# Kernel optimization log

Hardware: AMD Instinct MI355X
Metric: run time of the kernel (lower is better)

The kernel has to match this reference:

```python
import jax, jax.numpy as jnp
import numpy as np
from itertools import combinations

EPS = 1e-5

# flattened channel-pair index list: 36 pairs of the 9 GLCM shift channels -> 72 indices
PAIRS = np.asarray(list(combinations(range(9), 2)), dtype=np.int32).reshape(-1)


def glcm_stack(img):
    # img: [B,1,H,W]; replicate torch slice+cat shifts exactly (edge rows/cols duplicated)
    left = lambda a: jnp.concatenate([a[:, :, :, 1:], a[:, :, :, -1:]], axis=3)
    up = lambda a: jnp.concatenate([a[:, :, 1:, :], a[:, :, -1:, :]], axis=2)
    down = lambda a: jnp.concatenate([a[:, :, :1, :], a[:, :, :-1, :]], axis=2)
    right = lambda a: jnp.concatenate([a[:, :, :, :1], a[:, :, :, :-1]], axis=3)
    gl3, gl6, gl7, gl8 = left(img), up(img), down(img), down(img)
    return jnp.concatenate([
        img, left(img), up(img), up(gl3), right(img),
        down(img), left(gl6), left(gl7), right(gl8)], axis=1)  # [B,9,H,W]


def bn(x, gamma, beta, mean, var):
    scale = (gamma / jnp.sqrt(var + EPS))[:, None, None]
    return (x - mean[:, None, None]) * scale + beta[:, None, None]


def setup_inputs() -> dict:
    key = jax.random.key(0)
    ks = jax.random.split(key, 8)
    n = 36
    x = jax.random.normal(ks[0], (32, 64, 224, 224), dtype=jnp.float32)
    gw = jax.random.normal(ks[1], (n, 2), dtype=jnp.float32) * 0.5      # grouped 1x1 conv [out=n, in/group=2]
    w1 = jax.random.normal(ks[2], (n, n), dtype=jnp.float32) * 0.1      # 1x1 conv n->n
    ca_w1 = jax.random.normal(ks[3], (n // 2, n), dtype=jnp.float32) * 0.2
    ca_w2 = jax.random.normal(ks[4], (n, n // 2), dtype=jnp.float32) * 0.2
    bng_g = jnp.ones((n,), jnp.float32); bng_b = jnp.zeros((n,), jnp.float32)
    bng_m = jax.random.normal(ks[5], (n,), dtype=jnp.float32) * 0.1
    bng_v = jnp.abs(jax.random.normal(ks[6], (n,), dtype=jnp.float32)) + 0.5
    bn1_g = jnp.ones((n,), jnp.float32); bn1_b = jnp.zeros((n,), jnp.float32)
    bn1_m = jax.random.normal(ks[7], (n,), dtype=jnp.float32) * 0.1
    bn1_v = jnp.ones((n,), jnp.float32)
    return dict(x=x, gw=gw, w1=w1, ca_w1=ca_w1, ca_w2=ca_w2,
                bng_g=bng_g, bng_b=bng_b, bng_m=bng_m, bng_v=bng_v,
                bn1_g=bn1_g, bn1_b=bn1_b, bn1_m=bn1_m, bn1_v=bn1_v)


def reference(x, gw, w1, ca_w1, ca_w2, bng_g, bng_b, bng_m, bng_v,
              bn1_g, bn1_b, bn1_m, bn1_v):
    avgout = jnp.mean(x, axis=1, keepdims=True)            # [B,1,H,W]
    g = glcm_stack(avgout)                                 # [B,9,H,W]
    B, _, H, W = g.shape
    feas = jnp.take(g, jnp.asarray(PAIRS), axis=1)         # [B,72,H,W]
    feas = feas.reshape(B, 36, 2, H, W)
    y = jnp.einsum('bgchw,gc->bghw', feas, gw)             # grouped 1x1 conv
    y = jax.nn.relu(bn(y, bng_g, bng_b, bng_m, bng_v))
    y = jnp.einsum('bchw,oc->bohw', y, w1)                 # 1x1 conv n->n
    y = bn(y, bn1_g, bn1_b, bn1_m, bn1_v)
    pooled = jnp.mean(y, axis=(2, 3))                      # [B,36]
    att = jax.nn.sigmoid(jax.nn.relu(pooled @ ca_w1.T) @ ca_w2.T)  # [B,36]
    y = y * att[:, :, None, None]
    out = jax.nn.sigmoid(jnp.sum(y, axis=1, keepdims=True))  # [B,1,H,W]
    return out
```

## Files before the change

### kernel.cpp

```cpp
#include <hip/hip_runtime.h>
#include <math.h>

#define B_   32
#define C_   64
#define H_   224
#define W_   224
#define HW_  (H_*W_)
#define HW4_ (HW_/4)
#define G_   36
#define CHUNKS_ 28
#define PIX_PER_CHUNK_ (HW_/CHUNKS_)
#define PIX_PER_THREAD_ (PIX_PER_CHUNK_/256)

typedef float f4v __attribute__((ext_vector_type(4)));

__global__ __launch_bounds__(256) void k_mean(const float* __restrict__ x,
                                              float* __restrict__ a) {
    int b = blockIdx.x / 49;
    int i = (blockIdx.x % 49) * 256 + threadIdx.x;
    const f4v* x4 = reinterpret_cast<const f4v*>(x) + (size_t)b * C_ * HW4_ + i;
    f4v s = {0.f, 0.f, 0.f, 0.f};
    #pragma unroll 8
    for (int c = 0; c < C_; ++c) {
        s += x4[(size_t)c * HW4_];
    }
    s *= (1.0f / 64.0f);
    reinterpret_cast<f4v*>(a)[(size_t)b * HW4_ + i] = s;
}

__device__ __forceinline__ void gather9s(const float* __restrict__ ab, int p,
        float& n0, float& n1, float& n2, float& n3, float& n4,
        float& n5, float& n6, float& n7, float& n8) {
    int h = p / W_, w = p - (p / W_) * W_;
    int hm = h > 0 ? h - 1 : 0, hp = h < H_-1 ? h + 1 : H_-1;
    int wm = w > 0 ? w - 1 : 0, wp = w < W_-1 ? w + 1 : W_-1;
    n0 = ab[h*W_ + w];
    n1 = ab[h*W_ + wp];
    n2 = ab[hp*W_ + w];
    n3 = ab[hp*W_ + wp];
    n4 = ab[h*W_ + wm];
    n5 = ab[hm*W_ + w];
    n6 = n3;
    n7 = ab[hm*W_ + wp];
    n8 = ab[hm*W_ + wm];
}

#define PAIR_LIST(OP) \
  OP(0,0,1) OP(1,0,2) OP(2,0,3) OP(3,0,4) OP(4,0,5) OP(5,0,6) OP(6,0,7) OP(7,0,8) \
  OP(8,1,2) OP(9,1,3) OP(10,1,4) OP(11,1,5) OP(12,1,6) OP(13,1,7) OP(14,1,8) \
  OP(15,2,3) OP(16,2,4) OP(17,2,5) OP(18,2,6) OP(19,2,7) OP(20,2,8) \
  OP(21,3,4) OP(22,3,5) OP(23,3,6) OP(24,3,7) OP(25,3,8) \
  OP(26,4,5) OP(27,4,6) OP(28,4,7) OP(29,4,8) \
  OP(30,5,6) OP(31,5,7) OP(32,5,8) \
  OP(33,6,7) OP(34,6,8) OP(35,7,8)

__global__ __launch_bounds__(256) void k_sums(const float* __restrict__ a,
                                              const float* __restrict__ gw,
                                              const float* __restrict__ bng_g, const float* __restrict__ bng_b,
                                              const float* __restrict__ bng_m, const float* __restrict__ bng_v,
                                              float* __restrict__ partial) {
    int b = blockIdx.x / CHUNKS_;
    int chunk = blockIdx.x % CHUNKS_;
    int t = threadIdx.x;
    __shared__ float sA0[G_], sA1[G_], sB[G_];
    __shared__ float red[4 * G_];
    if (t < G_) {
        float sg = bng_g[t] / sqrtf(bng_v[t] + 1e-5f);
        sA0[t] = gw[2*t+0] * sg;
        sA1[t] = gw[2*t+1] * sg;
        sB[t]  = bng_b[t] - bng_m[t] * sg;
    }
    __syncthreads();
    const float* ab = a + (size_t)b * HW_;
    float acc[G_];
    #pragma unroll
    for (int g = 0; g < G_; ++g) acc[g] = 0.f;

    #pragma unroll 2
    for (int k = 0; k < PIX_PER_THREAD_; ++k) {
        int p = chunk * PIX_PER_CHUNK_ + k * 256 + t;
        float n0,n1,n2,n3,n4,n5,n6,n7,n8;
        gather9s(ab, p, n0,n1,n2,n3,n4,n5,n6,n7,n8);
        #define SUM_OP(g, i0, i1) { \
            float y = fmaf(sA0[g], n##i0, fmaf(sA1[g], n##i1, sB[g])); \
            acc[g] += fmaxf(y, 0.f); }
        PAIR_LIST(SUM_OP)
        #undef SUM_OP
    }

    int lane = t & 63, wave = t >> 6;
    #pragma unroll
    for (int g = 0; g < G_; ++g) {
        float v = acc[g];
        v += __shfl_down(v, 32);
        v += __shfl_down(v, 16);
        v += __shfl_down(v, 8);
        v += __shfl_down(v, 4);
        v += __shfl_down(v, 2);
        v += __shfl_down(v, 1);
        if (lane == 0) red[wave * G_ + g] = v;
    }
    __syncthreads();
    if (t < G_) {
        partial[(size_t)(b * CHUNKS_ + chunk) * G_ + t] =
            red[t] + red[G_+t] + red[2*G_+t] + red[3*G_+t];
    }
}

__global__ void k_att(const float* __restrict__ partial,
                      const float* __restrict__ bn1_g, const float* __restrict__ bn1_b,
                      const float* __restrict__ bn1_m, const float* __restrict__ bn1_v,
                      const float* __restrict__ w1, const float* __restrict__ ca_w1,
                      const float* __restrict__ ca_w2,
                      float* __restrict__ vout, float* __restrict__ cout) {
    int b = blockIdx.x;
    int t = threadIdx.x;
    __shared__ float ss1[G_], sb1[G_];
    __shared__ float meanr[G_], pooled[G_], hid[G_/2], att[G_];
    if (t < G_) {
        float s1 = bn1_g[t] / sqrtf(bn1_v[t] + 1e-5f);
        ss1[t] = s1;
        sb1[t] = bn1_b[t] - bn1_m[t] * s1;
        float s = 0.f;
        for (int j = 0; j < CHUNKS_; ++j) s += partial[(size_t)(b * CHUNKS_ + j) * G_ + t];
        meanr[t] = s * (1.0f / (float)HW_);
    }
    __syncthreads();
    if (t < G_) {
        float s = 0.f;
        #pragma unroll
        for (int g = 0; g < G_; ++g) s += w1[t*G_ + g] * meanr[g];
        pooled[t] = fmaf(s, ss1[t], sb1[t]);
    }
    __syncthreads();
    if (t < G_/2) {
        float s = 0.f;
        #pragma unroll
        for (int o = 0; o < G_; ++o) s += pooled[o] * ca_w1[t*G_ + o];
        hid[t] = fmaxf(s, 0.f);
    }
    __syncthreads();
    if (t < G_) {
        float s = 0.f;
        #pragma unroll
        for (int k = 0; k < G_/2; ++k) s += hid[k] * ca_w2[t*(G_/2) + k];
        att[t] = 1.0f / (1.0f + expf(-s));
    }
    __syncthreads();
    if (t < G_) {
        float s = 0.f;
        #pragma unroll
        for (int o = 0; o < G_; ++o) s += att[o] * ss1[o] * w1[o*G_ + t];
        vout[b*G_ + t] = s;
    }
    if (t == 63) {
        float s = 0.f;
        #pragma unroll
        for (int o = 0; o < G_; ++o) s += att[o] * sb1[o];
        cout[b] = s;
    }
}

__global__ __launch_bounds__(256) void k_out(const float* __restrict__ a,
                                             const float* __restrict__ gw,
                                             const float* __restrict__ bng_g, const float* __restrict__ bng_b,
                                             const float* __restrict__ bng_m, const float* __restrict__ bng_v,
                                             const float* __restrict__ v,
                                             const float* __restrict__ cvals,
                                             float* __restrict__ out) {
    int b = blockIdx.x / CHUNKS_;
    int chunk = blockIdx.x % CHUNKS_;
    int t = threadIdx.x;
    __shared__ float sA0[G_], sA1[G_], sB[G_], sV[G_];
    __shared__ float sC;
    if (t < G_) {
        float sg = bng_g[t] / sqrtf(bng_v[t] + 1e-5f);
        sA0[t] = gw[2*t+0] * sg;
        sA1[t] = gw[2*t+1] * sg;
        sB[t]  = bng_b[t] - bng_m[t] * sg;
        sV[t]  = v[b*G_ + t];
    }
    if (t == 63) sC = cvals[b];
    __syncthreads();
    const float* ab = a + (size_t)b * HW_;
    float* ob = out + (size_t)b * HW_;
    #pragma unroll 2
    for (int k = 0; k < PIX_PER_THREAD_; ++k) {
        int p = chunk * PIX_PER_CHUNK_ + k * 256 + t;
        float n0,n1,n2,n3,n4,n5,n6,n7,n8;
        gather9s(ab, p, n0,n1,n2,n3,n4,n5,n6,n7,n8);
        float s = sC;
        #define OUT_OP(g, i0, i1) { \
            float y = fmaf(sA0[g], n##i0, fmaf(sA1[g], n##i1, sB[g])); \
            s = fmaf(fmaxf(y, 0.f), sV[g], s); }
        PAIR_LIST(OUT_OP)
        #undef OUT_OP
        ob[p] = 1.0f / (1.0f + expf(-s));
    }
}

extern "C" void kernel_launch(void* const* d_in, const int* in_sizes, int n_in,
                              void* d_out, int out_size, void* d_ws, size_t ws_size,
                              hipStream_t stream) {
    const float* x     = (const float*)d_in[0];
    const float* gw    = (const float*)d_in[1];
    const float* w1    = (const float*)d_in[2];
    const float* ca_w1 = (const float*)d_in[3];
    const float* ca_w2 = (const float*)d_in[4];
    const float* bng_g = (const float*)d_in[5];
    const float* bng_b = (const float*)d_in[6];
    const float* bng_m = (const float*)d_in[7];
    const float* bng_v = (const float*)d_in[8];
    const float* bn1_g = (const float*)d_in[9];
    const float* bn1_b = (const float*)d_in[10];
    const float* bn1_m = (const float*)d_in[11];
    const float* bn1_v = (const float*)d_in[12];

    float* ws      = (float*)d_ws;
    float* a       = ws;
    float* partial = a + (size_t)B_ * HW_;
    float* v       = partial + (size_t)B_ * CHUNKS_ * G_;
    float* cvals   = v + B_ * G_;

    k_mean<<<B_ * 49, 256, 0, stream>>>(x, a);
    k_sums<<<B_ * CHUNKS_, 256, 0, stream>>>(a, gw,
        bng_g, bng_b, bng_m, bng_v, partial);
    k_att<<<B_, 64, 0, stream>>>(partial,
        bn1_g, bn1_b, bn1_m, bn1_v, w1, ca_w1, ca_w2, v, cvals);
    k_out<<<B_ * CHUNKS_, 256, 0, stream>>>(a, gw,
        bng_g, bng_b, bng_m, bng_v, v, cvals, (float*)d_out);
}
```

Before: 127.0 us.

## Fuse channel mean with pair-sum pass using shared-memory row bands

The channel-mean kernel and the ReLU pair-sum kernel are merged. Each block averages the 64 channels for an 8-row band, keeps the band in shared memory and computes the 36 pair sums for the 6 interior rows from it. A new small kernel computes the band-boundary rows, which need neighbours from other bands, by reading the global mean buffer. This removes one separate pass over the mean map in exchange for an extra launch and a fused kernel with fewer blocks during the bandwidth-heavy mean phase, where some threads sit idle.

```diff
diff --git a/kernel.cpp b/kernel.cpp
--- a/kernel.cpp
+++ b/kernel.cpp
@@ -11,22 +11,19 @@
 #define CHUNKS_ 28
 #define PIX_PER_CHUNK_ (HW_/CHUNKS_)
 #define PIX_PER_THREAD_ (PIX_PER_CHUNK_/256)
+#define ROWS_PER_BAND_ 8
+#define EDGE_BLOCKS_ 7
 
 typedef float f4v __attribute__((ext_vector_type(4)));
 
-__global__ __launch_bounds__(256) void k_mean(const float* __restrict__ x,
-                                              float* __restrict__ a) {
-    int b = blockIdx.x / 49;
-    int i = (blockIdx.x % 49) * 256 + threadIdx.x;
-    const f4v* x4 = reinterpret_cast<const f4v*>(x) + (size_t)b * C_ * HW4_ + i;
-    f4v s = {0.f, 0.f, 0.f, 0.f};
-    #pragma unroll 8
-    for (int c = 0; c < C_; ++c) {
-        s += x4[(size_t)c * HW4_];
-    }
-    s *= (1.0f / 64.0f);
-    reinterpret_cast<f4v*>(a)[(size_t)b * HW4_ + i] = s;
-}
+#define PAIR_LIST(OP) \
+  OP(0,0,1) OP(1,0,2) OP(2,0,3) OP(3,0,4) OP(4,0,5) OP(5,0,6) OP(6,0,7) OP(7,0,8) \
+  OP(8,1,2) OP(9,1,3) OP(10,1,4) OP(11,1,5) OP(12,1,6) OP(13,1,7) OP(14,1,8) \
+  OP(15,2,3) OP(16,2,4) OP(17,2,5) OP(18,2,6) OP(19,2,7) OP(20,2,8) \
+  OP(21,3,4) OP(22,3,5) OP(23,3,6) OP(24,3,7) OP(25,3,8) \
+  OP(26,4,5) OP(27,4,6) OP(28,4,7) OP(29,4,8) \
+  OP(30,5,6) OP(31,5,7) OP(32,5,8) \
+  OP(33,6,7) OP(34,6,8) OP(35,7,8)
 
 __device__ __forceinline__ void gather9s(const float* __restrict__ ab, int p,
         float& n0, float& n1, float& n2, float& n3, float& n4,
@@ -45,24 +42,18 @@
     n8 = ab[hm*W_ + wm];
 }
 
-#define PAIR_LIST(OP) \
-  OP(0,0,1) OP(1,0,2) OP(2,0,3) OP(3,0,4) OP(4,0,5) OP(5,0,6) OP(6,0,7) OP(7,0,8) \
-  OP(8,1,2) OP(9,1,3) OP(10,1,4) OP(11,1,5) OP(12,1,6) OP(13,1,7) OP(14,1,8) \
-  OP(15,2,3) OP(16,2,4) OP(17,2,5) OP(18,2,6) OP(19,2,7) OP(20,2,8) \
-  OP(21,3,4) OP(22,3,5) OP(23,3,6) OP(24,3,7) OP(25,3,8) \
-  OP(26,4,5) OP(27,4,6) OP(28,4,7) OP(29,4,8) \
-  OP(30,5,6) OP(31,5,7) OP(32,5,8) \
-  OP(33,6,7) OP(34,6,8) OP(35,7,8)
-
-__global__ __launch_bounds__(256) void k_sums(const float* __restrict__ a,
-                                              const float* __restrict__ gw,
-                                              const float* __restrict__ bng_g, const float* __restrict__ bng_b,
-                                              const float* __restrict__ bng_m, const float* __restrict__ bng_v,
-                                              float* __restrict__ partial) {
+__global__ __launch_bounds__(256) void k_mean_sums(
+        const float* __restrict__ x, float* __restrict__ a,
+        const float* __restrict__ gw,
+        const float* __restrict__ bng_g, const float* __restrict__ bng_b,
+        const float* __restrict__ bng_m, const float* __restrict__ bng_v,
+        float* __restrict__ partial) {
     int b = blockIdx.x / CHUNKS_;
     int chunk = blockIdx.x % CHUNKS_;
+    int r0 = chunk * ROWS_PER_BAND_;
     int t = threadIdx.x;
     __shared__ float sA0[G_], sA1[G_], sB[G_];
+    __shared__ float smean[ROWS_PER_BAND_ * W_];
     __shared__ float red[4 * G_];
     if (t < G_) {
         float sg = bng_g[t] / sqrtf(bng_v[t] + 1e-5f);
@@ -70,24 +61,46 @@
         sA1[t] = gw[2*t+1] * sg;
         sB[t]  = bng_b[t] - bng_m[t] * sg;
     }
-    __syncthreads();
-    const float* ab = a + (size_t)b * HW_;
+    const f4v* xb = reinterpret_cast<const f4v*>(x) + (size_t)b * C_ * HW4_;
+    f4v* ab4 = reinterpret_cast<f4v*>(a) + (size_t)b * HW4_;
+    #pragma unroll 1
+    for (int k = 0; k < 2; ++k) {
+        int q = k * 256 + t;
+        if (q < ROWS_PER_BAND_ * (W_/4)) {
+            int off = r0 * (W_/4) + q;
+            const f4v* xp = xb + off;
+            f4v s = {0.f, 0.f, 0.f, 0.f};
+            #pragma unroll 8
+            for (int c = 0; c < C_; ++c) s += xp[(size_t)c * HW4_];
+            s *= (1.0f / 64.0f);
+            ab4[off] = s;
+            *reinterpret_cast<f4v*>(&smean[q * 4]) = s;
+        }
+    }
+    __syncthreads();
     float acc[G_];
     #pragma unroll
     for (int g = 0; g < G_; ++g) acc[g] = 0.f;
-
-    #pragma unroll 2
-    for (int k = 0; k < PIX_PER_THREAD_; ++k) {
-        int p = chunk * PIX_PER_CHUNK_ + k * 256 + t;
-        float n0,n1,n2,n3,n4,n5,n6,n7,n8;
-        gather9s(ab, p, n0,n1,n2,n3,n4,n5,n6,n7,n8);
-        #define SUM_OP(g, i0, i1) { \
-            float y = fmaf(sA0[g], n##i0, fmaf(sA1[g], n##i1, sB[g])); \
-            acc[g] += fmaxf(y, 0.f); }
-        PAIR_LIST(SUM_OP)
-        #undef SUM_OP
-    }
-
+    #pragma unroll 1
+    for (int k = 0; k < 6; ++k) {
+        int q = k * 256 + t;
+        if (q < 6 * W_) {
+            int row = 1 + q / W_;
+            int col = q - (q / W_) * W_;
+            int wm = col > 0 ? col - 1 : 0;
+            int wp = col < W_-1 ? col + 1 : W_-1;
+            const float* rC = &smean[row * W_];
+            const float* rU = &smean[(row-1) * W_];
+            const float* rD = &smean[(row+1) * W_];
+            float n0 = rC[col], n1 = rC[wp], n2 = rD[col], n3 = rD[wp],
+                  n4 = rC[wm], n5 = rU[col], n6 = n3, n7 = rU[wp], n8 = rU[wm];
+            #define SUM_OP(g, i0, i1) { \
+                float y = fmaf(sA0[g], n##i0, fmaf(sA1[g], n##i1, sB[g])); \
+                acc[g] += fmaxf(y, 0.f); }
+            PAIR_LIST(SUM_OP)
+            #undef SUM_OP
+        }
+    }
     int lane = t & 63, wave = t >> 6;
     #pragma unroll
     for (int g = 0; g < G_; ++g) {
@@ -107,7 +120,64 @@
     }
 }
 
+__global__ __launch_bounds__(256) void k_edge(
+        const float* __restrict__ a,
+        const float* __restrict__ gw,
+        const float* __restrict__ bng_g, const float* __restrict__ bng_b,
+        const float* __restrict__ bng_m, const float* __restrict__ bng_v,
+        float* __restrict__ partial2) {
+    int b = blockIdx.x / EDGE_BLOCKS_;
+    int j = blockIdx.x % EDGE_BLOCKS_;
+    int t = threadIdx.x;
+    __shared__ float sA0[G_], sA1[G_], sB[G_];
+    __shared__ float red[4 * G_];
+    if (t < G_) {
+        float sg = bng_g[t] / sqrtf(bng_v[t] + 1e-5f);
+        sA0[t] = gw[2*t+0] * sg;
+        sA1[t] = gw[2*t+1] * sg;
+        sB[t]  = bng_b[t] - bng_m[t] * sg;
+    }
+    __syncthreads();
+    const float* ab = a + (size_t)b * HW_;
+    float acc[G_];
+    #pragma unroll
+    for (int g = 0; g < G_; ++g) acc[g] = 0.f;
+    #pragma unroll 1
+    for (int k = 0; k < 7; ++k) {
+        int q = k * 256 + t;
+        int lrow = q / W_;
+        int col = q - lrow * W_;
+        int i = j * 8 + lrow;
+        int r = 4 * i + 3 * (i & 1);
+        float n0,n1,n2,n3,n4,n5,n6,n7,n8;
+        gather9s(ab, r * W_ + col, n0,n1,n2,n3,n4,n5,n6,n7,n8);
+        #define SUM_OP(g, i0, i1) { \
+            float y = fmaf(sA0[g], n##i0, fmaf(sA1[g], n##i1, sB[g])); \
+            acc[g] += fmaxf(y, 0.f); }
+        PAIR_LIST(SUM_OP)
+        #undef SUM_OP
+    }
+    int lane = t & 63, wave = t >> 6;
+    #pragma unroll
+    for (int g = 0; g < G_; ++g) {
+        float v = acc[g];
+        v += __shfl_down(v, 32);
+        v += __shfl_down(v, 16);
+        v += __shfl_down(v, 8);
+        v += __shfl_down(v, 4);
+        v += __shfl_down(v, 2);
+        v += __shfl_down(v, 1);
+        if (lane == 0) red[wave * G_ + g] = v;
+    }
+    __syncthreads();
+    if (t < G_) {
+        partial2[(size_t)(b * EDGE_BLOCKS_ + j) * G_ + t] =
+            red[t] + red[G_+t] + red[2*G_+t] + red[3*G_+t];
+    }
+}
+
 __global__ void k_att(const float* __restrict__ partial,
+                      const float* __restrict__ partial2,
                       const float* __restrict__ bn1_g, const float* __restrict__ bn1_b,
                       const float* __restrict__ bn1_m, const float* __restrict__ bn1_v,
                       const float* __restrict__ w1, const float* __restrict__ ca_w1,
@@ -123,6 +193,7 @@
         sb1[t] = bn1_b[t] - bn1_m[t] * s1;
         float s = 0.f;
         for (int j = 0; j < CHUNKS_; ++j) s += partial[(size_t)(b * CHUNKS_ + j) * G_ + t];
+        for (int j = 0; j < EDGE_BLOCKS_; ++j) s += partial2[(size_t)(b * EDGE_BLOCKS_ + j) * G_ + t];
         meanr[t] = s * (1.0f / (float)HW_);
     }
     __syncthreads();
@@ -216,16 +287,18 @@
     const float* bn1_m = (const float*)d_in[11];
     const float* bn1_v = (const float*)d_in[12];
 
-    float* ws      = (float*)d_ws;
-    float* a       = ws;
-    float* partial = a + (size_t)B_ * HW_;
-    float* v       = partial + (size_t)B_ * CHUNKS_ * G_;
-    float* cvals   = v + B_ * G_;
-
-    k_mean<<<B_ * 49, 256, 0, stream>>>(x, a);
-    k_sums<<<B_ * CHUNKS_, 256, 0, stream>>>(a, gw,
+    float* ws       = (float*)d_ws;
+    float* a        = ws;
+    float* partial  = a + (size_t)B_ * HW_;
+    float* partial2 = partial + (size_t)B_ * CHUNKS_ * G_;
+    float* v        = partial2 + (size_t)B_ * EDGE_BLOCKS_ * G_;
+    float* cvals    = v + B_ * G_;
+
+    k_mean_sums<<<B_ * CHUNKS_, 256, 0, stream>>>(x, a, gw,
         bng_g, bng_b, bng_m, bng_v, partial);
-    k_att<<<B_, 64, 0, stream>>>(partial,
+    k_edge<<<B_ * EDGE_BLOCKS_, 256, 0, stream>>>(a, gw,
+        bng_g, bng_b, bng_m, bng_v, partial2);
+    k_att<<<B_, 64, 0, stream>>>(partial, partial2,
         bn1_g, bn1_b, bn1_m, bn1_v, w1, ca_w1, ca_w2, v, cvals);
     k_out<<<B_ * CHUNKS_, 256, 0, stream>>>(a, gw,
         bng_g, bng_b, bng_m, bng_v, v, cvals, (float*)d_out);
```

After: 132.2 us. 4.1% more time.

## Stage row bands in LDS and slide a register window for stencil passes

Applied to the files above, without the earlier changes.

Both the partial-sum and output kernels now load a 10-row band (8 rows plus halo) of the averaged image into shared memory with vectorized loads. Each thread then walks 7 consecutive pixels of one row, reusing neighbor values from a sliding register window instead of doing 8 scattered global loads with per-pixel div/mod. Per-group constants are hoisted into registers. This cuts redundant global/L2 traffic and index math, at the cost of more registers and LDS use and non-coalesced output stores of stride 7 per thread.

```diff
diff --git a/kernel.cpp b/kernel.cpp
--- a/kernel.cpp
+++ b/kernel.cpp
@@ -9,8 +9,8 @@
 #define HW4_ (HW_/4)
 #define G_   36
 #define CHUNKS_ 28
-#define PIX_PER_CHUNK_ (HW_/CHUNKS_)
-#define PIX_PER_THREAD_ (PIX_PER_CHUNK_/256)
+#define ROWS_ 8
+#define SEGW_ 7
 
 typedef float f4v __attribute__((ext_vector_type(4)));
 
@@ -28,23 +28,6 @@
     reinterpret_cast<f4v*>(a)[(size_t)b * HW4_ + i] = s;
 }
 
-__device__ __forceinline__ void gather9s(const float* __restrict__ ab, int p,
-        float& n0, float& n1, float& n2, float& n3, float& n4,
-        float& n5, float& n6, float& n7, float& n8) {
-    int h = p / W_, w = p - (p / W_) * W_;
-    int hm = h > 0 ? h - 1 : 0, hp = h < H_-1 ? h + 1 : H_-1;
-    int wm = w > 0 ? w - 1 : 0, wp = w < W_-1 ? w + 1 : W_-1;
-    n0 = ab[h*W_ + w];
-    n1 = ab[h*W_ + wp];
-    n2 = ab[hp*W_ + w];
-    n3 = ab[hp*W_ + wp];
-    n4 = ab[h*W_ + wm];
-    n5 = ab[hm*W_ + w];
-    n6 = n3;
-    n7 = ab[hm*W_ + wp];
-    n8 = ab[hm*W_ + wm];
-}
-
 #define PAIR_LIST(OP) \
   OP(0,0,1) OP(1,0,2) OP(2,0,3) OP(3,0,4) OP(4,0,5) OP(5,0,6) OP(6,0,7) OP(7,0,8) \
   OP(8,1,2) OP(9,1,3) OP(10,1,4) OP(11,1,5) OP(12,1,6) OP(13,1,7) OP(14,1,8) \
@@ -53,6 +36,21 @@
   OP(26,4,5) OP(27,4,6) OP(28,4,7) OP(29,4,8) \
   OP(30,5,6) OP(31,5,7) OP(32,5,8) \
   OP(33,6,7) OP(34,6,8) OP(35,7,8)
+
+#define STAGE_BAND() do { \
+    const f4v* ab4 = reinterpret_cast<const f4v*>(a + (size_t)b * HW_); \
+    _Pragma("unroll") \
+    for (int k = 0; k < 3; ++k) { \
+        int q = k * 256 + t; \
+        if (q < 10 * (W_/4)) { \
+            int row = q / (W_/4); \
+            int c4  = q - row * (W_/4); \
+            int gr = r0 - 1 + row; \
+            gr = gr < 0 ? 0 : (gr > H_-1 ? H_-1 : gr); \
+            *reinterpret_cast<f4v*>(&sm[row * W_ + c4 * 4]) = ab4[gr * (W_/4) + c4]; \
+        } \
+    } } while (0)
+
 
 __global__ __launch_bounds__(256) void k_sums(const float* __restrict__ a,
                                               const float* __restrict__ gw,
@@ -63,6 +61,7 @@
     int chunk = blockIdx.x % CHUNKS_;
     int t = threadIdx.x;
     __shared__ float sA0[G_], sA1[G_], sB[G_];
+    __shared__ float sm[10 * W_];
     __shared__ float red[4 * G_];
     if (t < G_) {
         float sg = bng_g[t] / sqrtf(bng_v[t] + 1e-5f);
@@ -70,36 +69,45 @@
         sA1[t] = gw[2*t+1] * sg;
         sB[t]  = bng_b[t] - bng_m[t] * sg;
     }
-    __syncthreads();
-    const float* ab = a + (size_t)b * HW_;
-    float acc[G_];
+    int r0 = chunk * ROWS_;
+    STAGE_BAND();
+    __syncthreads();
+
+    int seg = t & 31, lr = t >> 5;
+    int w0 = seg * SEGW_;
+    const float* RU = &sm[lr * W_];
+    const float* RC = &sm[(lr+1) * W_];
+    const float* RD = &sm[(lr+2) * W_];
+
+    #define LOADC(g,i0,i1) float A0##g = sA0[g], A1##g = sA1[g], Bc##g = sB[g];
+    PAIR_LIST(LOADC)
+    #undef LOADC
+    #define DECLACC(g,i0,i1) float acc##g = 0.f;
+    PAIR_LIST(DECLACC)
+    #undef DECLACC
+
+    int cI = w0 > 0 ? w0 - 1 : 0;
+    float uL = RU[cI], cl_ = RC[cI];
+    float uC = RU[w0], cc_ = RC[w0], dC = RD[w0];
     #pragma unroll
-    for (int g = 0; g < G_; ++g) acc[g] = 0.f;
-
-    #pragma unroll 2
-    for (int k = 0; k < PIX_PER_THREAD_; ++k) {
-        int p = chunk * PIX_PER_CHUNK_ + k * 256 + t;
-        float n0,n1,n2,n3,n4,n5,n6,n7,n8;
-        gather9s(ab, p, n0,n1,n2,n3,n4,n5,n6,n7,n8);
-        #define SUM_OP(g, i0, i1) { \
-            float y = fmaf(sA0[g], n##i0, fmaf(sA1[g], n##i1, sB[g])); \
-            acc[g] += fmaxf(y, 0.f); }
+    for (int j = 0; j < SEGW_; ++j) {
+        int cR = w0 + j + 1; cR = cR < W_ ? cR : W_ - 1;
+        float uR = RU[cR], cr_ = RC[cR], dR = RD[cR];
+        float n0 = cc_, n1 = cr_, n2 = dC, n3 = dR, n4 = cl_,
+              n5 = uC, n6 = dR, n7 = uR, n8 = uL;
+        #define SUM_OP(g,i0,i1) acc##g += fmaxf(fmaf(A0##g, n##i0, fmaf(A1##g, n##i1, Bc##g)), 0.f);
         PAIR_LIST(SUM_OP)
         #undef SUM_OP
+        uL = uC; cl_ = cc_; uC = uR; cc_ = cr_; dC = dR;
     }
 
     int lane = t & 63, wave = t >> 6;
-    #pragma unroll
-    for (int g = 0; g < G_; ++g) {
-        float v = acc[g];
-        v += __shfl_down(v, 32);
-        v += __shfl_down(v, 16);
-        v += __shfl_down(v, 8);
-        v += __shfl_down(v, 4);
-        v += __shfl_down(v, 2);
-        v += __shfl_down(v, 1);
-        if (lane == 0) red[wave * G_ + g] = v;
-    }
+    #define RED_OP(g,i0,i1) { float v = acc##g; \
+        v += __shfl_down(v, 32); v += __shfl_down(v, 16); v += __shfl_down(v, 8); \
+        v += __shfl_down(v, 4);  v += __shfl_down(v, 2);  v += __shfl_down(v, 1); \
+        if (lane == 0) red[wave * G_ + g] = v; }
+    PAIR_LIST(RED_OP)
+    #undef RED_OP
     __syncthreads();
     if (t < G_) {
         partial[(size_t)(b * CHUNKS_ + chunk) * G_ + t] =
@@ -172,6 +180,7 @@
     int chunk = blockIdx.x % CHUNKS_;
     int t = threadIdx.x;
     __shared__ float sA0[G_], sA1[G_], sB[G_], sV[G_];
+    __shared__ float sm[10 * W_];
     __shared__ float sC;
     if (t < G_) {
         float sg = bng_g[t] / sqrtf(bng_v[t] + 1e-5f);
@@ -181,21 +190,37 @@
         sV[t]  = v[b*G_ + t];
     }
     if (t == 63) sC = cvals[b];
-    __syncthreads();
-    const float* ab = a + (size_t)b * HW_;
-    float* ob = out + (size_t)b * HW_;
-    #pragma unroll 2
-    for (int k = 0; k < PIX_PER_THREAD_; ++k) {
-        int p = chunk * PIX_PER_CHUNK_ + k * 256 + t;
-        float n0,n1,n2,n3,n4,n5,n6,n7,n8;
-        gather9s(ab, p, n0,n1,n2,n3,n4,n5,n6,n7,n8);
-        float s = sC;
-        #define OUT_OP(g, i0, i1) { \
-            float y = fmaf(sA0[g], n##i0, fmaf(sA1[g], n##i1, sB[g])); \
-            s = fmaf(fmaxf(y, 0.f), sV[g], s); }
+    int r0 = chunk * ROWS_;
+    STAGE_BAND();
+    __syncthreads();
+
+    int seg = t & 31, lr = t >> 5;
+    int w0 = seg * SEGW_;
+    const float* RU = &sm[lr * W_];
+    const float* RC = &sm[(lr+1) * W_];
+    const float* RD = &sm[(lr+2) * W_];
+    float* ob = out + (size_t)b * HW_ + (r0 + lr) * W_;
+
+    #define LOADC(g,i0,i1) float A0##g = sA0[g], A1##g = sA1[g], Bc##g = sB[g], V##g = sV[g];
+    PAIR_LIST(LOADC)
+    #undef LOADC
+    float c0 = sC;
+
+    int cI = w0 > 0 ? w0 - 1 : 0;
+    float uL = RU[cI], cl_ = RC[cI];
+    float uC = RU[w0], cc_ = RC[w0], dC = RD[w0];
+    #pragma unroll
+    for (int j = 0; j < SEGW_; ++j) {
+        int cR = w0 + j + 1; cR = cR < W_ ? cR : W_ - 1;
+        float uR = RU[cR], cr_ = RC[cR], dR = RD[cR];
+        float n0 = cc_, n1 = cr_, n2 = dC, n3 = dR, n4 = cl_,
+              n5 = uC, n6 = dR, n7 = uR, n8 = uL;
+        float s = c0;
+        #define OUT_OP(g,i0,i1) s = fmaf(fmaxf(fmaf(A0##g, n##i0, fmaf(A1##g, n##i1, Bc##g)), 0.f), V##g, s);
         PAIR_LIST(OUT_OP)
         #undef OUT_OP
-        ob[p] = 1.0f / (1.0f + expf(-s));
+        ob[w0 + j] = 1.0f / (1.0f + expf(-s));
+        uL = uC; cl_ = cc_; uC = uR; cc_ = cr_; dC = dR;
     }
 }
 
```

Measured after the change: 121.6 us. -4.3%, faster.
